# Performance work log

Hardware: AMD Instinct MI355X
Metric: run time of the kernel (lower is better)

The kernel has to match this reference:

```python
import jax, jax.numpy as jnp
import numpy as np

# Config constants (from CantorFusionConfigV2 defaults / init_kwargs)
NUM_HEADS = 8
HEAD_DIM = 64
K_NEIGHBORS = 64        # fusion_window
LEVELS = 5              # k_simplex + 1
TAU = 0.25
BASE = 3.0
ALPHA = 0.5
EPS = 1e-8
RESIDUAL_SCALE = 1.0


def _cantor_measure(S):
    """Vectorized Devil's Staircase Cantor measure for S positions in [0,1]. Returns [S]."""
    pos = (jnp.arange(S, dtype=jnp.float32) + 0.5) / S
    pos = jnp.clip(pos, 1e-10, 1.0 - 1e-10)
    ks = jnp.arange(1, LEVELS + 1, dtype=jnp.float32)
    scales = BASE ** ks                      # [L]
    lvl_w = 0.5 ** ks                        # [L]
    centers = jnp.array([0.5, 1.5, 2.5], dtype=jnp.float32)
    y = jnp.mod(pos[:, None] * scales, BASE)            # [S, L]
    logits = -((y[..., None] - centers) ** 2) / (TAU + 1e-10)  # [S, L, 3]
    p = jax.nn.softmax(logits, axis=-1)
    bits = p[..., 2] + ALPHA * p[..., 1]                # [S, L]
    return jnp.sum(bits * lvl_w, axis=-1)               # [S]


def _routes_and_weights(S):
    """KNN routes [S,K] by Cantor distance + inverse-distance softmax weights [S,K]."""
    cm = _cantor_measure(S)
    Dm = jnp.abs(cm[:, None] - cm[None, :])             # [S, S]
    Dm = Dm / (Dm.max() + 1e-10)
    neg_d, routes = jax.lax.top_k(-Dm, K_NEIGHBORS)     # k smallest distances
    route_dist = -neg_d                                  # [S, K]
    w = jax.nn.softmax(1.0 / (route_dist + EPS), axis=-1)
    return routes, w


def setup_inputs() -> dict:
    key = jax.random.key(0)
    k1, k2, k3 = jax.random.split(key, 3)
    B, S, D = 2, 2048, 512
    x = jax.random.normal(k1, (B, S, D), dtype=jnp.float32)
    W_in = jax.random.normal(k2, (D, D), dtype=jnp.float32) * (1.0 / np.sqrt(D))
    b_in = jnp.zeros((D,), dtype=jnp.float32)
    W_out = jax.random.normal(k3, (D, D), dtype=jnp.float32) * (1.0 / np.sqrt(D))
    b_out = jnp.zeros((D,), dtype=jnp.float32)
    return {"x": x, "W_in": W_in, "b_in": b_in, "W_out": W_out, "b_out": b_out}


def reference(x, W_in, b_in, W_out, b_out):
    B, S, dim = x.shape
    routes, w = _routes_and_weights(S)                   # [S,K], [S,K] (no-grad geometry)
    routes = jax.lax.stop_gradient(routes)
    w = jax.lax.stop_gradient(w)
    # input projection and head split -> [B, H, S, D]
    h = (x @ W_in + b_in).reshape(B, S, NUM_HEADS, HEAD_DIM).transpose(0, 2, 1, 3)
    # neighbor gather [B, H, S, K, D] then inverse-distance weighted sum
    gathered = h[:, :, routes, :]                        # [B,H,S,K,D]
    fused = jnp.einsum('bhskd,sk->bhsd', gathered, w)    # [B,H,S,D]
    out = fused.transpose(0, 2, 1, 3).reshape(B, S, dim) @ W_out + b_out
    return x + RESIDUAL_SCALE * out
```

## Files before the change

kernel.cpp:

```cpp
#include <hip/hip_runtime.h>
#include <hip/hip_bf16.h>

#define S_LEN 2048
#define K_NB  64

typedef __attribute__((ext_vector_type(8))) short bf16x8;
typedef __attribute__((ext_vector_type(4))) float f32x4;
typedef __attribute__((ext_vector_type(4))) unsigned int u32x4;

__device__ inline unsigned short f2b(float f) {
    unsigned u = __builtin_bit_cast(unsigned, f);
    return (unsigned short)((u + 0x7FFFu + ((u >> 16) & 1u)) >> 16);
}

__device__ inline int swoff(int row, int k) {
    int o = row * 128 + k * 2;
    return o ^ ((row & 7) << 4);
}

__global__ __launch_bounds__(256) void prep_kernel(
    const float* __restrict__ W_in, const float* __restrict__ W_out,
    const float* __restrict__ b_in, const float* __restrict__ b_out,
    unsigned short* __restrict__ Wb_in, unsigned short* __restrict__ Wt_out,
    float* __restrict__ cmf, float* __restrict__ bc) {
    int b = blockIdx.x, tid = threadIdx.x;
    if (b < 128) {
        int base = (b * 256 + tid) * 8;
        float4 v0 = *(const float4*)(W_in + base);
        float4 v1 = *(const float4*)(W_in + base + 4);
        unsigned short t[8] = { f2b(v0.x), f2b(v0.y), f2b(v0.z), f2b(v0.w),
                                f2b(v1.x), f2b(v1.y), f2b(v1.z), f2b(v1.w) };
        *(u32x4*)(Wb_in + base) = *(u32x4*)t;
    } else if (b < 256) {
        int u = (b - 128) * 256 + tid;
        int n = u & 511, kc = (u >> 9) * 8;
        unsigned short t[8];
        #pragma unroll
        for (int j = 0; j < 8; ++j) t[j] = f2b(W_out[(size_t)(kc + j) * 512 + n]);
        *(u32x4*)(Wt_out + (size_t)n * 512 + kc) = *(u32x4*)t;
    } else if (b < 264) {
        int s = (b - 256) * 256 + tid;
        float pos = ((float)s + 0.5f) * (1.0f / 2048.0f);
        float cm = 0.0f, scale = 1.0f, lvlw = 1.0f;
        #pragma unroll
        for (int k = 1; k <= 5; ++k) {
            scale *= 3.0f; lvlw *= 0.5f;
            float y = fmodf(pos * scale, 3.0f);
            float d0 = y - 0.5f, d1 = y - 1.5f, d2 = y - 2.5f;
            float l0 = -(d0 * d0) * 4.0f;
            float l1 = -(d1 * d1) * 4.0f;
            float l2 = -(d2 * d2) * 4.0f;
            float m = fmaxf(l0, fmaxf(l1, l2));
            float e0 = (float)exp((double)(l0 - m));
            float e1 = (float)exp((double)(l1 - m));
            float e2 = (float)exp((double)(l2 - m));
            float sum = (e0 + e1) + e2;
            float p1 = e1 / sum, p2 = e2 / sum;
            cm += (p2 + 0.5f * p1) * lvlw;
        }
        cmf[s] = cm;
    } else {
        __shared__ float red[4][64];
        int bb = b - 264;
        int nl = tid & 63, jc = tid >> 6;
        int n = bb * 64 + nl;
        float acc = 0.0f;
        #pragma unroll 8
        for (int j = jc * 128; j < jc * 128 + 128; ++j)
            acc += b_in[j] * W_out[(size_t)j * 512 + n];
        red[jc][nl] = acc;
        __syncthreads();
        if (jc == 0)
            bc[n] = b_out[n] + ((red[0][nl] + red[1][nl]) +
                                (red[2][nl] + red[3][nl]));
    }
}

__global__ __launch_bounds__(256) void mid_kernel(
    const float* __restrict__ cmf, int* __restrict__ routes,
    int* __restrict__ counts,
    const unsigned short* __restrict__ Wt_out,
    const unsigned short* __restrict__ Wb_in,
    unsigned short* __restrict__ Wct) {
    __shared__ char lds[(64 + 128) * 64 * 2];
    int b = blockIdx.x, tid = threadIdx.x;
    int wid = tid >> 6, lane = tid & 63;
    if (b < 32) {
        char* As = lds;
        char* Bs = lds + 64 * 64 * 2;
        int bm = b >> 2, bn = b & 3;
        int wr = wid >> 1, wc = wid & 1;
        int l15 = lane & 15, l4 = lane >> 4;
        int arow = tid >> 2, akq = (tid & 3) * 16;
        int brow = tid >> 1, bkh = (tid & 1) * 32;
        const unsigned short* asrc = Wt_out + (size_t)(bm * 64 + arow) * 512 + akq;
        const unsigned short* bsrc = Wb_in + (size_t)(bn * 128 + brow) * 512 + bkh;
        u32x4 arg[2], brg[4];
        auto la = [&](int k0) {
            arg[0] = *(const u32x4*)(asrc + k0);
            arg[1] = *(const u32x4*)(asrc + k0 + 8);
        };
        auto lb = [&](int k0) {
            #pragma unroll
            for (int i = 0; i < 4; ++i) brg[i] = *(const u32x4*)(bsrc + k0 + i * 8);
        };
        f32x4 acc[2][4] = {};
        la(0); lb(0);
        for (int k0 = 0; k0 < 512; k0 += 64) {
            *(u32x4*)(As + swoff(arow, akq))     = arg[0];
            *(u32x4*)(As + swoff(arow, akq + 8)) = arg[1];
            #pragma unroll
            for (int i = 0; i < 4; ++i)
                *(u32x4*)(Bs + swoff(brow, bkh + i * 8)) = brg[i];
            __syncthreads();
            if (k0 + 64 < 512) { la(k0 + 64); lb(k0 + 64); }
            #pragma unroll
            for (int kk = 0; kk < 2; ++kk) {
                const int kb = kk * 32 + l4 * 8;
                bf16x8 af[2], bg[4];
                #pragma unroll
                for (int m = 0; m < 2; ++m)
                    af[m] = *(bf16x8*)(As + swoff(wr * 32 + m * 16 + l15, kb));
                #pragma unroll
                for (int n = 0; n < 4; ++n)
                    bg[n] = *(bf16x8*)(Bs + swoff(wc * 64 + n * 16 + l15, kb));
                #pragma unroll
                for (int m = 0; m < 2; ++m)
                    #pragma unroll
                    for (int n = 0; n < 4; ++n)
                        acc[m][n] = __builtin_amdgcn_mfma_f32_16x16x32_bf16(
                            af[m], bg[n], acc[m][n], 0, 0, 0);
            }
            __syncthreads();
        }
        #pragma unroll
        for (int m = 0; m < 2; ++m)
            #pragma unroll
            for (int r = 0; r < 4; ++r) {
                int row = bm * 64 + wr * 32 + m * 16 + l4 * 4 + r;
                #pragma unroll
                for (int n = 0; n < 4; ++n) {
                    int col = bn * 128 + wc * 64 + n * 16 + l15;
                    Wct[(size_t)row * 512 + col] = f2b(acc[m][n][r]);
                }
            }
    } else {
        int s = (b - 32) * 4 + wid;
        float v = cmf[s];
        int n = 0;
        int* rt = routes + s * K_NB;
        for (int j0 = 0; j0 < S_LEN; j0 += 64) {
            float c = cmf[j0 + lane];
            bool m = (c == v);
            unsigned long long mask = __ballot(m);
            if (m) {
                int idx = n + __popcll(mask & ((1ull << lane) - 1ull));
                if (idx < K_NB) rt[idx] = j0 + lane;
            }
            n += __popcll(mask);
        }
        if (lane == 0) counts[s] = n < K_NB ? n : K_NB;
    }
}

__global__ __launch_bounds__(256) void avgx_kernel(
    const float* __restrict__ x, const int* __restrict__ routes,
    const int* __restrict__ counts, unsigned short* __restrict__ xa) {
    int tid = threadIdx.x;
    int row = blockIdx.x * 16 + (tid >> 4);
    int c0 = (tid & 15) * 32;
    int s = row & (S_LEN - 1), bidx = row >> 11;
    int gn = counts[s];
    unsigned short* dst = xa + (size_t)row * 512 + c0;
    unsigned short t[32];
    if (gn == 1) {
        const float* p = x + (size_t)row * 512 + c0;
        #pragma unroll
        for (int i = 0; i < 8; ++i) {
            float4 v = *(const float4*)(p + i * 4);
            t[i*4+0] = f2b(v.x); t[i*4+1] = f2b(v.y);
            t[i*4+2] = f2b(v.z); t[i*4+3] = f2b(v.w);
        }
    } else {
        const int* rt = routes + s * K_NB;
        const float* xb = x + (size_t)bidx * S_LEN * 512 + c0;
        float av[32] = {};
        for (int e = 0; e < gn; ++e) {
            const float* p = xb + (size_t)rt[e] * 512;
            #pragma unroll
            for (int i = 0; i < 8; ++i) {
                float4 v = *(const float4*)(p + i * 4);
                av[i*4+0] += v.x; av[i*4+1] += v.y;
                av[i*4+2] += v.z; av[i*4+3] += v.w;
            }
        }
        float ginv = 1.0f / (float)gn;
        #pragma unroll
        for (int i = 0; i < 32; ++i) t[i] = f2b(av[i] * ginv);
    }
    #pragma unroll
    for (int i = 0; i < 4; ++i)
        *(u32x4*)(dst + i * 8) = *(u32x4*)&t[i * 8];
}

__global__ __launch_bounds__(256) void gemmF_kernel(
    const float* __restrict__ x, const unsigned short* __restrict__ xa,
    const unsigned short* __restrict__ Wct, const float* __restrict__ bc,
    float* __restrict__ out) {
    __shared__ char lds[2 * 64 * 64 * 2];
    char* As = lds;
    char* Bs = lds + 64 * 64 * 2;
    const int tid = threadIdx.x;
    const int id = blockIdx.x;
    const int xcd = id & 7, slot = id >> 3;
    const int bm = xcd * 8 + (slot & 7);
    const int bn = slot >> 3;
    const int wid = tid >> 6, lane = tid & 63;
    const int wr = wid >> 1, wc = wid & 1;
    const int l15 = lane & 15, l4 = lane >> 4;
    const int arow = tid >> 2, akq = (tid & 3) * 16;

    const unsigned short* asrc = xa  + (size_t)(bm * 64 + arow) * 512 + akq;
    const unsigned short* bsrc = Wct + (size_t)(bn * 64 + arow) * 512 + akq;

    u32x4 arg[2], brg[2];
    auto la = [&](int k0) {
        arg[0] = *(const u32x4*)(asrc + k0);
        arg[1] = *(const u32x4*)(asrc + k0 + 8);
    };
    auto lb = [&](int k0) {
        brg[0] = *(const u32x4*)(bsrc + k0);
        brg[1] = *(const u32x4*)(bsrc + k0 + 8);
    };

    f32x4 acc[2][2] = {};
    la(0); lb(0);
    for (int k0 = 0; k0 < 512; k0 += 64) {
        *(u32x4*)(As + swoff(arow, akq))     = arg[0];
        *(u32x4*)(As + swoff(arow, akq + 8)) = arg[1];
        *(u32x4*)(Bs + swoff(arow, akq))     = brg[0];
        *(u32x4*)(Bs + swoff(arow, akq + 8)) = brg[1];
        __syncthreads();
        if (k0 + 64 < 512) { la(k0 + 64); lb(k0 + 64); }
        #pragma unroll
        for (int kk = 0; kk < 2; ++kk) {
            const int kb = kk * 32 + l4 * 8;
            bf16x8 af[2], bg[2];
            #pragma unroll
            for (int m = 0; m < 2; ++m)
                af[m] = *(bf16x8*)(As + swoff(wr * 32 + m * 16 + l15, kb));
            #pragma unroll
            for (int n = 0; n < 2; ++n)
                bg[n] = *(bf16x8*)(Bs + swoff(wc * 32 + n * 16 + l15, kb));
            #pragma unroll
            for (int m = 0; m < 2; ++m)
                #pragma unroll
                for (int n = 0; n < 2; ++n)
                    acc[m][n] = __builtin_amdgcn_mfma_f32_16x16x32_bf16(
                        af[m], bg[n], acc[m][n], 0, 0, 0);
        }
        __syncthreads();
    }

    float bv[2];
    #pragma unroll
    for (int n = 0; n < 2; ++n) bv[n] = bc[bn * 64 + wc * 32 + n * 16 + l15];
    #pragma unroll
    for (int m = 0; m < 2; ++m)
        #pragma unroll
        for (int r = 0; r < 4; ++r) {
            int row = bm * 64 + wr * 32 + m * 16 + l4 * 4 + r;
            #pragma unroll
            for (int n = 0; n < 2; ++n) {
                int col = bn * 64 + wc * 32 + n * 16 + l15;
                float v = acc[m][n][r] + bv[n];
                out[(size_t)row * 512 + col] = x[(size_t)row * 512 + col] + v;
            }
        }
}

extern "C" void kernel_launch(void* const* d_in, const int* in_sizes, int n_in,
                              void* d_out, int out_size, void* d_ws, size_t ws_size,
                              hipStream_t stream) {
    const float* x     = (const float*)d_in[0];
    const float* W_in  = (const float*)d_in[1];
    const float* b_in  = (const float*)d_in[2];
    const float* W_out = (const float*)d_in[3];
    const float* b_out = (const float*)d_in[4];
    float* out = (float*)d_out;

    char* ws = (char*)d_ws;
    float*          cmf    = (float*)ws;
    int*            counts = (int*)(ws + 8192);
    int*            routes = (int*)(ws + 16384);
    unsigned short* Wb_in  = (unsigned short*)(ws + 16384 + 524288);
    unsigned short* Wt_out = (unsigned short*)(ws + 16384 + 2 * 524288);
    unsigned short* Wct    = (unsigned short*)(ws + 16384 + 3 * 524288);
    float*          bc     = (float*)(ws + 16384 + 4 * 524288);
    unsigned short* xa     = (unsigned short*)(ws + 16384 + 4 * 524288 + 4096);

    prep_kernel<<<272, 256, 0, stream>>>(W_in, W_out, b_in, b_out,
                                         Wb_in, Wt_out, cmf, bc);
    mid_kernel<<<544, 256, 0, stream>>>(cmf, routes, counts,
                                        Wt_out, Wb_in, Wct);
    avgx_kernel<<<256, 256, 0, stream>>>(x, routes, counts, xa);
    gemmF_kernel<<<512, 256, 0, stream>>>(x, xa, Wct, bc, out);
}
```

Before: 34.59 us.

## Fuse weight prep, route search and neighbor averaging into one combo kernel

Restructures the four-launch pipeline into three launches. The small Cantor-measure computation gets its own kernel. A single combo kernel then computes the folded weight product directly from fp32 W_in/W_out with on-the-fly bf16 conversion, computes the bias, and does route search plus neighbor averaging per row using LDS-cached cantor values. This removes the intermediate bf16 weight copies, the routes/counts buffers and one launch. In exchange the weight GEMM loses its register prefetch, reads W_out with strided column loads, and averaging now loops over all group members even for singleton groups.

```diff
diff --git a/kernel.cpp b/kernel.cpp
--- a/kernel.cpp
+++ b/kernel.cpp
@@ -2,7 +2,6 @@
 #include <hip/hip_bf16.h>
 
 #define S_LEN 2048
-#define K_NB  64
 
 typedef __attribute__((ext_vector_type(8))) short bf16x8;
 typedef __attribute__((ext_vector_type(4))) float f32x4;
@@ -18,50 +17,102 @@
     return o ^ ((row & 7) << 4);
 }
 
-__global__ __launch_bounds__(256) void prep_kernel(
+__global__ __launch_bounds__(256) void cantor_kernel(float* __restrict__ cmf) {
+    int s = blockIdx.x * 256 + threadIdx.x;
+    float pos = ((float)s + 0.5f) * (1.0f / 2048.0f);
+    float cm = 0.0f, scale = 1.0f, lvlw = 1.0f;
+    #pragma unroll
+    for (int k = 1; k <= 5; ++k) {
+        scale *= 3.0f; lvlw *= 0.5f;
+        float y = fmodf(pos * scale, 3.0f);
+        float d0 = y - 0.5f, d1 = y - 1.5f, d2 = y - 2.5f;
+        float l0 = -(d0 * d0) * 4.0f;
+        float l1 = -(d1 * d1) * 4.0f;
+        float l2 = -(d2 * d2) * 4.0f;
+        float m = fmaxf(l0, fmaxf(l1, l2));
+        float e0 = (float)exp((double)(l0 - m));
+        float e1 = (float)exp((double)(l1 - m));
+        float e2 = (float)exp((double)(l2 - m));
+        float sum = (e0 + e1) + e2;
+        float p1 = e1 / sum, p2 = e2 / sum;
+        cm += (p2 + 0.5f * p1) * lvlw;
+    }
+    cmf[s] = cm;
+}
+
+__global__ __launch_bounds__(256) void combo_kernel(
+    const float* __restrict__ x,
     const float* __restrict__ W_in, const float* __restrict__ W_out,
     const float* __restrict__ b_in, const float* __restrict__ b_out,
-    unsigned short* __restrict__ Wb_in, unsigned short* __restrict__ Wt_out,
-    float* __restrict__ cmf, float* __restrict__ bc) {
-    int b = blockIdx.x, tid = threadIdx.x;
-    if (b < 128) {
-        int base = (b * 256 + tid) * 8;
-        float4 v0 = *(const float4*)(W_in + base);
-        float4 v1 = *(const float4*)(W_in + base + 4);
-        unsigned short t[8] = { f2b(v0.x), f2b(v0.y), f2b(v0.z), f2b(v0.w),
-                                f2b(v1.x), f2b(v1.y), f2b(v1.z), f2b(v1.w) };
-        *(u32x4*)(Wb_in + base) = *(u32x4*)t;
-    } else if (b < 256) {
-        int u = (b - 128) * 256 + tid;
-        int n = u & 511, kc = (u >> 9) * 8;
-        unsigned short t[8];
-        #pragma unroll
-        for (int j = 0; j < 8; ++j) t[j] = f2b(W_out[(size_t)(kc + j) * 512 + n]);
-        *(u32x4*)(Wt_out + (size_t)n * 512 + kc) = *(u32x4*)t;
-    } else if (b < 264) {
-        int s = (b - 256) * 256 + tid;
-        float pos = ((float)s + 0.5f) * (1.0f / 2048.0f);
-        float cm = 0.0f, scale = 1.0f, lvlw = 1.0f;
-        #pragma unroll
-        for (int k = 1; k <= 5; ++k) {
-            scale *= 3.0f; lvlw *= 0.5f;
-            float y = fmodf(pos * scale, 3.0f);
-            float d0 = y - 0.5f, d1 = y - 1.5f, d2 = y - 2.5f;
-            float l0 = -(d0 * d0) * 4.0f;
-            float l1 = -(d1 * d1) * 4.0f;
-            float l2 = -(d2 * d2) * 4.0f;
-            float m = fmaxf(l0, fmaxf(l1, l2));
-            float e0 = (float)exp((double)(l0 - m));
-            float e1 = (float)exp((double)(l1 - m));
-            float e2 = (float)exp((double)(l2 - m));
-            float sum = (e0 + e1) + e2;
-            float p1 = e1 / sum, p2 = e2 / sum;
-            cm += (p2 + 0.5f * p1) * lvlw;
-        }
-        cmf[s] = cm;
-    } else {
-        __shared__ float red[4][64];
-        int bb = b - 264;
+    const float* __restrict__ cmf,
+    unsigned short* __restrict__ Wct, float* __restrict__ bc,
+    unsigned short* __restrict__ xa) {
+    __shared__ char lds[24576];
+    const int b = blockIdx.x, tid = threadIdx.x;
+    const int wid = tid >> 6, lane = tid & 63;
+
+    if (b < 32) {
+        char* As = lds;
+        char* Bs = lds + 8192;
+        int bm = b >> 2, bn = b & 3;
+        int wr = wid >> 1, wc = wid & 1;
+        int l15 = lane & 15, l4 = lane >> 4;
+        int an = tid & 63, ajg = tid >> 6;
+        int bk = tid >> 1, bjh = (tid & 1) * 32;
+        const float* acol = W_out + bm * 64 + an;
+        const float* brow = W_in + (size_t)(bn * 128 + bk) * 512 + bjh;
+        f32x4 acc[2][4] = {};
+        for (int k0 = 0; k0 < 512; k0 += 64) {
+            unsigned short ta[16];
+            #pragma unroll
+            for (int i = 0; i < 16; ++i)
+                ta[i] = f2b(acol[(size_t)(k0 + ajg * 16 + i) * 512]);
+            *(u32x4*)(As + swoff(an, ajg * 16))     = *(u32x4*)&ta[0];
+            *(u32x4*)(As + swoff(an, ajg * 16 + 8)) = *(u32x4*)&ta[8];
+            unsigned short tb[32];
+            #pragma unroll
+            for (int i = 0; i < 8; ++i) {
+                float4 v = *(const float4*)(brow + k0 + i * 4);
+                tb[i*4+0] = f2b(v.x); tb[i*4+1] = f2b(v.y);
+                tb[i*4+2] = f2b(v.z); tb[i*4+3] = f2b(v.w);
+            }
+            #pragma unroll
+            for (int i = 0; i < 4; ++i)
+                *(u32x4*)(Bs + swoff(bk, bjh + i * 8)) = *(u32x4*)&tb[i*8];
+            __syncthreads();
+            #pragma unroll
+            for (int kk = 0; kk < 2; ++kk) {
+                const int kb = kk * 32 + l4 * 8;
+                bf16x8 af[2], bg[4];
+                #pragma unroll
+                for (int m = 0; m < 2; ++m)
+                    af[m] = *(bf16x8*)(As + swoff(wr * 32 + m * 16 + l15, kb));
+                #pragma unroll
+                for (int n = 0; n < 4; ++n)
+                    bg[n] = *(bf16x8*)(Bs + swoff(wc * 64 + n * 16 + l15, kb));
+                #pragma unroll
+                for (int m = 0; m < 2; ++m)
+                    #pragma unroll
+                    for (int n = 0; n < 4; ++n)
+                        acc[m][n] = __builtin_amdgcn_mfma_f32_16x16x32_bf16(
+                            af[m], bg[n], acc[m][n], 0, 0, 0);
+            }
+            __syncthreads();
+        }
+        #pragma unroll
+        for (int m = 0; m < 2; ++m)
+            #pragma unroll
+            for (int r = 0; r < 4; ++r) {
+                int row = bm * 64 + wr * 32 + m * 16 + l4 * 4 + r;
+                #pragma unroll
+                for (int n = 0; n < 4; ++n) {
+                    int col = bn * 128 + wc * 64 + n * 16 + l15;
+                    Wct[(size_t)row * 512 + col] = f2b(acc[m][n][r]);
+                }
+            }
+    } else if (b < 40) {
+        float (*red)[64] = (float(*)[64])lds;
+        int bb = b - 32;
         int nl = tid & 63, jc = tid >> 6;
         int n = bb * 64 + nl;
         float acc = 0.0f;
@@ -73,134 +124,54 @@
         if (jc == 0)
             bc[n] = b_out[n] + ((red[0][nl] + red[1][nl]) +
                                 (red[2][nl] + red[3][nl]));
+    } else {
+        float* cml = (float*)lds;
+        int*   mem = (int*)(lds + 8192) + wid * 64;
+        for (int i = tid; i < 512; i += 256)
+            *(float4*)&cml[i * 4] = *(const float4*)&cmf[i * 4];
+        __syncthreads();
+        int gidx = b - 40;
+        #pragma unroll
+        for (int q = 0; q < 2; ++q) {
+            int s = gidx * 8 + wid * 2 + q;
+            float v = cml[s];
+            int n = 0;
+            for (int j0 = 0; j0 < S_LEN; j0 += 64) {
+                float c = cml[j0 + lane];
+                bool m = (c == v);
+                unsigned long long mask = __ballot(m);
+                if (m) {
+                    int idx = n + __popcll(mask & ((1ull << lane) - 1ull));
+                    if (idx < 64) mem[idx] = j0 + lane;
+                }
+                n += __popcll(mask);
+            }
+            int gn = n < 64 ? n : 64;
+            __syncthreads();
+            float a0[8] = {}, a1[8] = {};
+            for (int e = 0; e < gn; ++e) {
+                int r = mem[e];
+                const float* p0 = x + (size_t)r * 512 + lane * 8;
+                const float* p1 = p0 + (size_t)S_LEN * 512;
+                float4 u0 = *(const float4*)p0, u1 = *(const float4*)(p0 + 4);
+                float4 w0 = *(const float4*)p1, w1 = *(const float4*)(p1 + 4);
+                a0[0] += u0.x; a0[1] += u0.y; a0[2] += u0.z; a0[3] += u0.w;
+                a0[4] += u1.x; a0[5] += u1.y; a0[6] += u1.z; a0[7] += u1.w;
+                a1[0] += w0.x; a1[1] += w0.y; a1[2] += w0.z; a1[3] += w0.w;
+                a1[4] += w1.x; a1[5] += w1.y; a1[6] += w1.z; a1[7] += w1.w;
+            }
+            float gi = 1.0f / (float)gn;
+            unsigned short t0[8], t1[8];
+            #pragma unroll
+            for (int i = 0; i < 8; ++i) {
+                t0[i] = f2b(a0[i] * gi);
+                t1[i] = f2b(a1[i] * gi);
+            }
+            *(u32x4*)(xa + (size_t)s * 512 + lane * 8)           = *(u32x4*)t0;
+            *(u32x4*)(xa + (size_t)(S_LEN + s) * 512 + lane * 8) = *(u32x4*)t1;
+            __syncthreads();
+        }
     }
-}
-
-__global__ __launch_bounds__(256) void mid_kernel(
-    const float* __restrict__ cmf, int* __restrict__ routes,
-    int* __restrict__ counts,
-    const unsigned short* __restrict__ Wt_out,
-    const unsigned short* __restrict__ Wb_in,
-    unsigned short* __restrict__ Wct) {
-    __shared__ char lds[(64 + 128) * 64 * 2];
-    int b = blockIdx.x, tid = threadIdx.x;
-    int wid = tid >> 6, lane = tid & 63;
-    if (b < 32) {
-        char* As = lds;
-        char* Bs = lds + 64 * 64 * 2;
-        int bm = b >> 2, bn = b & 3;
-        int wr = wid >> 1, wc = wid & 1;
-        int l15 = lane & 15, l4 = lane >> 4;
-        int arow = tid >> 2, akq = (tid & 3) * 16;
-        int brow = tid >> 1, bkh = (tid & 1) * 32;
-        const unsigned short* asrc = Wt_out + (size_t)(bm * 64 + arow) * 512 + akq;
-        const unsigned short* bsrc = Wb_in + (size_t)(bn * 128 + brow) * 512 + bkh;
-        u32x4 arg[2], brg[4];
-        auto la = [&](int k0) {
-            arg[0] = *(const u32x4*)(asrc + k0);
-            arg[1] = *(const u32x4*)(asrc + k0 + 8);
-        };
-        auto lb = [&](int k0) {
-            #pragma unroll
-            for (int i = 0; i < 4; ++i) brg[i] = *(const u32x4*)(bsrc + k0 + i * 8);
-        };
-        f32x4 acc[2][4] = {};
-        la(0); lb(0);
-        for (int k0 = 0; k0 < 512; k0 += 64) {
-            *(u32x4*)(As + swoff(arow, akq))     = arg[0];
-            *(u32x4*)(As + swoff(arow, akq + 8)) = arg[1];
-            #pragma unroll
-            for (int i = 0; i < 4; ++i)
-                *(u32x4*)(Bs + swoff(brow, bkh + i * 8)) = brg[i];
-            __syncthreads();
-            if (k0 + 64 < 512) { la(k0 + 64); lb(k0 + 64); }
-            #pragma unroll
-            for (int kk = 0; kk < 2; ++kk) {
-                const int kb = kk * 32 + l4 * 8;
-                bf16x8 af[2], bg[4];
-                #pragma unroll
-                for (int m = 0; m < 2; ++m)
-                    af[m] = *(bf16x8*)(As + swoff(wr * 32 + m * 16 + l15, kb));
-                #pragma unroll
-                for (int n = 0; n < 4; ++n)
-                    bg[n] = *(bf16x8*)(Bs + swoff(wc * 64 + n * 16 + l15, kb));
-                #pragma unroll
-                for (int m = 0; m < 2; ++m)
-                    #pragma unroll
-                    for (int n = 0; n < 4; ++n)
-                        acc[m][n] = __builtin_amdgcn_mfma_f32_16x16x32_bf16(
-                            af[m], bg[n], acc[m][n], 0, 0, 0);
-            }
-            __syncthreads();
-        }
-        #pragma unroll
-        for (int m = 0; m < 2; ++m)
-            #pragma unroll
-            for (int r = 0; r < 4; ++r) {
-                int row = bm * 64 + wr * 32 + m * 16 + l4 * 4 + r;
-                #pragma unroll
-                for (int n = 0; n < 4; ++n) {
-                    int col = bn * 128 + wc * 64 + n * 16 + l15;
-                    Wct[(size_t)row * 512 + col] = f2b(acc[m][n][r]);
-                }
-            }
-    } else {
-        int s = (b - 32) * 4 + wid;
-        float v = cmf[s];
-        int n = 0;
-        int* rt = routes + s * K_NB;
-        for (int j0 = 0; j0 < S_LEN; j0 += 64) {
-            float c = cmf[j0 + lane];
-            bool m = (c == v);
-            unsigned long long mask = __ballot(m);
-            if (m) {
-                int idx = n + __popcll(mask & ((1ull << lane) - 1ull));
-                if (idx < K_NB) rt[idx] = j0 + lane;
-            }
-            n += __popcll(mask);
-        }
-        if (lane == 0) counts[s] = n < K_NB ? n : K_NB;
-    }
-}
-
-__global__ __launch_bounds__(256) void avgx_kernel(
-    const float* __restrict__ x, const int* __restrict__ routes,
-    const int* __restrict__ counts, unsigned short* __restrict__ xa) {
-    int tid = threadIdx.x;
-    int row = blockIdx.x * 16 + (tid >> 4);
-    int c0 = (tid & 15) * 32;
-    int s = row & (S_LEN - 1), bidx = row >> 11;
-    int gn = counts[s];
-    unsigned short* dst = xa + (size_t)row * 512 + c0;
-    unsigned short t[32];
-    if (gn == 1) {
-        const float* p = x + (size_t)row * 512 + c0;
-        #pragma unroll
-        for (int i = 0; i < 8; ++i) {
-            float4 v = *(const float4*)(p + i * 4);
-            t[i*4+0] = f2b(v.x); t[i*4+1] = f2b(v.y);
-            t[i*4+2] = f2b(v.z); t[i*4+3] = f2b(v.w);
-        }
-    } else {
-        const int* rt = routes + s * K_NB;
-        const float* xb = x + (size_t)bidx * S_LEN * 512 + c0;
-        float av[32] = {};
-        for (int e = 0; e < gn; ++e) {
-            const float* p = xb + (size_t)rt[e] * 512;
-            #pragma unroll
-            for (int i = 0; i < 8; ++i) {
-                float4 v = *(const float4*)(p + i * 4);
-                av[i*4+0] += v.x; av[i*4+1] += v.y;
-                av[i*4+2] += v.z; av[i*4+3] += v.w;
-            }
-        }
-        float ginv = 1.0f / (float)gn;
-        #pragma unroll
-        for (int i = 0; i < 32; ++i) t[i] = f2b(av[i] * ginv);
-    }
-    #pragma unroll
-    for (int i = 0; i < 4; ++i)
-        *(u32x4*)(dst + i * 8) = *(u32x4*)&t[i * 8];
 }
 
 __global__ __launch_bounds__(256) void gemmF_kernel(
@@ -290,19 +261,13 @@
     float* out = (float*)d_out;
 
     char* ws = (char*)d_ws;
-    float*          cmf    = (float*)ws;
-    int*            counts = (int*)(ws + 8192);
-    int*            routes = (int*)(ws + 16384);
-    unsigned short* Wb_in  = (unsigned short*)(ws + 16384 + 524288);
-    unsigned short* Wt_out = (unsigned short*)(ws + 16384 + 2 * 524288);
-    unsigned short* Wct    = (unsigned short*)(ws + 16384 + 3 * 524288);
-    float*          bc     = (float*)(ws + 16384 + 4 * 524288);
-    unsigned short* xa     = (unsigned short*)(ws + 16384 + 4 * 524288 + 4096);
-
-    prep_kernel<<<272, 256, 0, stream>>>(W_in, W_out, b_in, b_out,
-                                         Wb_in, Wt_out, cmf, bc);
-    mid_kernel<<<544, 256, 0, stream>>>(cmf, routes, counts,
-                                        Wt_out, Wb_in, Wct);
-    avgx_kernel<<<256, 256, 0, stream>>>(x, routes, counts, xa);
+    float*          cmf = (float*)ws;
+    unsigned short* Wct = (unsigned short*)(ws + 8192);
+    float*          bc  = (float*)(ws + 8192 + 524288);
+    unsigned short* xa  = (unsigned short*)(ws + 8192 + 524288 + 4096);
+
+    cantor_kernel<<<8, 256, 0, stream>>>(cmf);
+    combo_kernel<<<296, 256, 0, stream>>>(x, W_in, W_out, b_in, b_out,
+                                          cmf, Wct, bc, xa);
     gemmF_kernel<<<512, 256, 0, stream>>>(x, xa, Wct, bc, out);
 }
```

Result: slower. 35.94 us (+3.9%).
